# Performance work log

Measured on AMD Instinct MI355X. Metric: run time of the kernel, lower is better.

The kernel has to match this reference:

```python
import jax, jax.numpy as jnp
import numpy as np

EMB = 300; TOWERS = 6; LAYERS = 4; EPS = 1e-5; F_OUT = EMB // TOWERS  # 50
N_NODES = 3000; N_EDGES = 9000; N_GRAPHS = 64
NODE_VOCAB = 16; EDGE_VOCAB = 4


def _bn(x, g, b, m, v):
    # eval-mode BatchNorm1d with running stats
    return (x - m) * jax.lax.rsqrt(v + EPS) * g + b


def _forward(node_emb, edge_emb, W_edge, b_edge, W_pre, b_pre, W_post, b_post,
             W_lin, b_lin, bn_gamma, bn_beta, bn_mean, bn_var,
             head_w0, head_b0, gn0_gamma, gn0_beta, gn0_mean, gn0_var,
             head_w1, head_b1, gn1_gamma, gn1_beta, gn1_mean, gn1_var,
             head_w2, head_b2, x, edge_index, edge_attr, batch, num_graphs):
    N = x.shape[0]
    src, dst = edge_index[0], edge_index[1]
    h = node_emb[x]            # [N, D] node encoder (categorical embedding)
    e = edge_emb[edge_attr]    # [E, D] edge encoder
    cnt = jax.ops.segment_sum(jnp.ones(src.shape, h.dtype), dst, num_segments=N)
    deg = jnp.maximum(cnt, 1.0)
    log_deg = jnp.log(deg + 1.0)
    avg_log = jnp.mean(jnp.log(cnt + 1.0))  # PNA avg_deg['log'] of degree histogram
    amp = (log_deg / avg_log)[:, None, None]
    att = (avg_log / log_deg)[:, None, None]
    has_nb = (cnt > 0)[:, None, None]
    degc = deg[:, None, None]

    h_list = [h]
    for l in range(LAYERS):
        eproj = e @ W_edge[l] + b_edge[l]                        # [E, D]
        hcat = jnp.concatenate([h[dst], h[src], eproj], -1)      # [E, 3D] = [x_i, x_j, e]
        m = jnp.einsum('ef,tfd->etd', hcat, W_pre[l]) + b_pre[l]  # [E, T, D] per-tower pre-MLP
        s = jax.ops.segment_sum(m, dst, num_segments=N)
        mean = s / degc
        mn = jnp.where(has_nb, jax.ops.segment_min(m, dst, num_segments=N), 0.0)
        mx = jnp.where(has_nb, jax.ops.segment_max(m, dst, num_segments=N), 0.0)
        var = jax.ops.segment_sum(m * m, dst, num_segments=N) / degc - mean * mean
        std = jnp.sqrt(jax.nn.relu(var) + EPS)
        agg = jnp.concatenate([mean, mn, mx, std], -1)           # [N, T, 4D]
        agg = jnp.concatenate([agg, agg * amp, agg * att], -1)   # [N, T, 12D] scalers
        x_rep = jnp.broadcast_to(h[:, None, :], (N, TOWERS, EMB))
        post_in = jnp.concatenate([x_rep, agg], -1)              # [N, T, 13D]
        out = jnp.einsum('ntf,tfo->nto', post_in, W_post[l]) + b_post[l]  # [N, T, F_OUT]
        out = out.reshape(N, EMB) @ W_lin[l] + b_lin[l]
        out = _bn(out, bn_gamma[l], bn_beta[l], bn_mean[l], bn_var[l])
        if l < LAYERS - 1:
            out = jax.nn.relu(out)  # dropout is identity in eval mode
        h_list.append(out)
        h = out
    # JK='sum' exactly as in the original forward: sums h_list[0..num_layer-1]
    node_rep = h_list[0]
    for l in range(1, LAYERS):
        node_rep = node_rep + h_list[l]
    g = jax.ops.segment_sum(node_rep, batch, num_segments=num_graphs)  # global_add_pool
    g = jax.nn.relu(_bn(g @ head_w0 + head_b0, gn0_gamma, gn0_beta, gn0_mean, gn0_var))
    g = jax.nn.relu(_bn(g @ head_w1 + head_b1, gn1_gamma, gn1_beta, gn1_mean, gn1_var))
    return g @ head_w2 + head_b2


def setup_inputs() -> dict:
    key = jax.random.key(0)
    ks = jax.random.split(key, 16)
    D, T, L = EMB, TOWERS, LAYERS
    def rn(k, shape, s=0.05):
        return jax.random.normal(k, shape, dtype=jnp.float32) * s
    return {
        'x': jax.random.randint(ks[0], (N_NODES,), 0, NODE_VOCAB, dtype=jnp.int32),
        'edge_index': jax.random.randint(ks[1], (2, N_EDGES), 0, N_NODES, dtype=jnp.int32),
        'edge_attr': jax.random.randint(ks[2], (N_EDGES,), 0, EDGE_VOCAB, dtype=jnp.int32),
        'batch': jnp.sort(jax.random.randint(ks[3], (N_NODES,), 0, N_GRAPHS, dtype=jnp.int32)),
        'num_graphs': N_GRAPHS,
        'node_emb': rn(ks[4], (NODE_VOCAB, D), 1.0),
        'edge_emb': rn(ks[5], (EDGE_VOCAB, D), 1.0),
        'W_edge': rn(ks[6], (L, D, D)), 'b_edge': jnp.zeros((L, D), jnp.float32),
        'W_pre': rn(ks[7], (L, T, 3 * D, D)), 'b_pre': jnp.zeros((L, T, D), jnp.float32),
        'W_post': rn(ks[8], (L, T, 13 * D, F_OUT)), 'b_post': jnp.zeros((L, T, F_OUT), jnp.float32),
        'W_lin': rn(ks[9], (L, D, D)), 'b_lin': jnp.zeros((L, D), jnp.float32),
        'bn_gamma': jnp.ones((L, D), jnp.float32), 'bn_beta': jnp.zeros((L, D), jnp.float32),
        'bn_mean': jnp.zeros((L, D), jnp.float32), 'bn_var': jnp.ones((L, D), jnp.float32),
        'head_w0': rn(ks[10], (D, 2 * D)), 'head_b0': jnp.zeros((2 * D,), jnp.float32),
        'gn0_gamma': jnp.ones((2 * D,), jnp.float32), 'gn0_beta': jnp.zeros((2 * D,), jnp.float32),
        'gn0_mean': jnp.zeros((2 * D,), jnp.float32), 'gn0_var': jnp.ones((2 * D,), jnp.float32),
        'head_w1': rn(ks[11], (2 * D, D)), 'head_b1': jnp.zeros((D,), jnp.float32),
        'gn1_gamma': jnp.ones((D,), jnp.float32), 'gn1_beta': jnp.zeros((D,), jnp.float32),
        'gn1_mean': jnp.zeros((D,), jnp.float32), 'gn1_var': jnp.ones((D,), jnp.float32),
        'head_w2': rn(ks[12], (D, 1)), 'head_b2': jnp.zeros((1,), jnp.float32),
    }


def reference(x, edge_index, edge_attr, batch, num_graphs,
              node_emb, edge_emb, W_edge, b_edge, W_pre, b_pre, W_post, b_post,
              W_lin, b_lin, bn_gamma, bn_beta, bn_mean, bn_var,
              head_w0, head_b0, gn0_gamma, gn0_beta, gn0_mean, gn0_var,
              head_w1, head_b1, gn1_gamma, gn1_beta, gn1_mean, gn1_var,
              head_w2, head_b2):
    return _forward(node_emb, edge_emb, W_edge, b_edge, W_pre, b_pre, W_post, b_post,
                    W_lin, b_lin, bn_gamma, bn_beta, bn_mean, bn_var,
                    head_w0, head_b0, gn0_gamma, gn0_beta, gn0_mean, gn0_var,
                    head_w1, head_b1, gn1_gamma, gn1_beta, gn1_mean, gn1_var,
                    head_w2, head_b2, x, edge_index, edge_attr, batch, num_graphs)
```

## Files before the change

### kernel.cpp

```cpp
#include <hip/hip_runtime.h>
#include <math.h>

#define NN 3000
#define NE 9000
#define NG 64
#define D 300
#define NT 6
#define FO 50
#define EPSV 1e-5f
#define NB1 3900

__global__ void k_hist(const int* __restrict__ dst, int* __restrict__ cnt) {
    int e = blockIdx.x * blockDim.x + threadIdx.x;
    if (e < NE) atomicAdd(&cnt[dst[e]], 1);
}

__global__ __launch_bounds__(1024) void k_scan(
    const int* __restrict__ cnt, int* __restrict__ row_ptr, int* __restrict__ tmp_ptr,
    float* __restrict__ degf, float* __restrict__ ampv, float* __restrict__ attv) {
    __shared__ int s_part[1024];
    __shared__ float s_log[1024];
    int tid = threadIdx.x;
    int base = tid * 3;
    int c0 = 0, c1 = 0, c2 = 0; float lg = 0.f;
    if (base + 0 < NN) { c0 = cnt[base + 0]; lg += logf((float)c0 + 1.f); }
    if (base + 1 < NN) { c1 = cnt[base + 1]; lg += logf((float)c1 + 1.f); }
    if (base + 2 < NN) { c2 = cnt[base + 2]; lg += logf((float)c2 + 1.f); }
    s_part[tid] = c0 + c1 + c2;
    s_log[tid] = lg;
    __syncthreads();
    for (int off = 1; off < 1024; off <<= 1) {
        int v = (tid >= off) ? s_part[tid - off] : 0;
        __syncthreads();
        s_part[tid] += v;
        __syncthreads();
    }
    for (int off = 512; off > 0; off >>= 1) {
        if (tid < off) s_log[tid] += s_log[tid + off];
        __syncthreads();
    }
    float avg = s_log[0] / (float)NN;
    int run = (tid > 0) ? s_part[tid - 1] : 0;
    int cs[3] = {c0, c1, c2};
    for (int i = 0; i < 3; i++) {
        int n = base + i;
        if (n < NN) {
            row_ptr[n] = run; tmp_ptr[n] = run;
            int cc = cs[i];
            float dd = (float)(cc > 0 ? cc : 1);
            degf[n] = dd;
            float ld = logf(dd + 1.f);
            ampv[n] = ld / avg;
            attv[n] = avg / ld;
            run += cc;
        }
    }
    if (tid == 1023) row_ptr[NN] = s_part[1023];
}

__global__ void k_fill(const int* __restrict__ src, const int* __restrict__ dst,
                       const int* __restrict__ attr, int* __restrict__ tmp_ptr,
                       int2* __restrict__ edge_dat) {
    int e = blockIdx.x * blockDim.x + threadIdx.x;
    if (e < NE) {
        int d = dst[e];
        int p = atomicAdd(&tmp_ptr[d], 1);
        edge_dat[p] = make_int2(src[e], attr[e]);
    }
}

__global__ void k_embed(const int* __restrict__ x, const float* __restrict__ node_emb,
                        float* __restrict__ h, float* __restrict__ rep) {
    int i = blockIdx.x * blockDim.x + threadIdx.x;
    if (i < NN * D) {
        int n = i / D, d = i - n * D;
        float v = node_emb[x[n] * D + d];
        h[i] = v; rep[i] = v;
    }
}

__global__ void k_pack1(const float* __restrict__ W_pre, const float* __restrict__ W_post,
                        int l, float* __restrict__ Bp) {
    int idx = blockIdx.x * blockDim.x + threadIdx.x;
    if (idx >= 300 * NB1) return;
    int f = idx / NB1, j = idx - f * NB1;
    float v;
    if (j < 3600) {
        int s = j / 1800, r = j - s * 1800;
        int t = r / 300, d = r - t * 300;
        v = W_pre[(((size_t)(l * NT + t) * 900) + s * 300 + f) * 300 + d];
    } else {
        int jj = j - 3600;
        int t = jj / FO, o = jj - t * FO;
        v = W_post[((size_t)(l * NT + t) * 3900 + f) * FO + o];
    }
    Bp[idx] = v;
}

__global__ void k_packpost(const float* __restrict__ W_post, int l, float* __restrict__ Bp) {
    int idx = blockIdx.x * blockDim.x + threadIdx.x;
    if (idx >= NT * 1200 * 160) return;
    int t = idx / 192000, r = idx - t * 192000;
    int f = r / 160, c = r - f * 160;
    float v = 0.f;
    if (c < 150) {
        int k = c / FO, o = c - k * FO;
        v = W_post[((size_t)(l * NT + t) * 3900 + 300 + k * 1200 + f) * FO + o];
    }
    Bp[idx] = v;
}

__global__ void k_ep4(const float* __restrict__ edge_emb, const float* __restrict__ W_edge,
                      const float* __restrict__ b_edge, int l, float* __restrict__ ep4) {
    int idx = blockIdx.x * blockDim.x + threadIdx.x;
    if (idx >= 4 * 300) return;
    int a = idx / 300, f = idx - a * 300;
    float s = b_edge[l * 300 + f];
    for (int k = 0; k < 300; k++)
        s = fmaf(edge_emb[a * 300 + k], W_edge[((size_t)l * 300 + k) * 300 + f], s);
    ep4[idx] = s;
}

__global__ void k_ep_proj(const float* __restrict__ ep4, const float* __restrict__ W_pre,
                          const float* __restrict__ b_pre, int l, float* __restrict__ Ep) {
    int idx = blockIdx.x * blockDim.x + threadIdx.x;
    if (idx >= 4 * 1800) return;
    int a = idx / 1800, c = idx - a * 1800;
    int t = c / 300, d = c - t * 300;
    float s = b_pre[(l * NT + t) * 300 + d];
    for (int f = 0; f < 300; f++)
        s = fmaf(ep4[a * 300 + f], W_pre[(((size_t)(l * NT + t) * 900) + 600 + f) * 300 + d], s);
    Ep[idx] = s;
}

__global__ void k_pack_lin(const float* __restrict__ W_lin, const float* __restrict__ b_lin,
                           const float* __restrict__ gam, const float* __restrict__ bet,
                           const float* __restrict__ mu, const float* __restrict__ var,
                           int l, float* __restrict__ Wf, float* __restrict__ bf) {
    int idx = blockIdx.x * blockDim.x + threadIdx.x;
    if (idx >= 300 * 300) return;
    int f = idx / 300, j = idx - f * 300;
    float s = gam[l * 300 + j] * rsqrtf(var[l * 300 + j] + EPSV);
    Wf[idx] = W_lin[((size_t)l * 300 + f) * 300 + j] * s;
    if (f == 0) bf[j] = (b_lin[l * 300 + j] - mu[l * 300 + j]) * s + bet[l * 300 + j];
}

template <int EPI>
__global__ __launch_bounds__(256) void k_gemm(
    const float* __restrict__ A, int lda,
    const float* __restrict__ B, int ldb,
    float* __restrict__ C, int ldc,
    int M, int N, int K,
    const float* __restrict__ bias, float* __restrict__ rep,
    const float* __restrict__ gam, const float* __restrict__ bet,
    const float* __restrict__ mu, const float* __restrict__ var) {
    constexpr int BM = 64, BN = 64, BK = 16, LAS = BM + 4;
    __shared__ float As[BK * LAS];
    __shared__ float Bs[BK * BN];
    int tid = threadIdx.x;
    int tx = tid & 15, ty = tid >> 4;
    int bm = blockIdx.y * BM, bn = blockIdx.x * BN;
    int arow = tid >> 2;
    int akq = (tid & 3) * 4;
    int bj = tid & 63, bk0 = tid >> 6;
    float acc[4][4] = {};
    for (int k0 = 0; k0 < K; k0 += BK) {
        {
            float4 av = make_float4(0.f, 0.f, 0.f, 0.f);
            int grow = bm + arow;
            if (grow < M) {
                int gk = k0 + akq;
                if (gk + 3 < K) {
                    av = *(const float4*)&A[(size_t)grow * lda + gk];
                } else {
                    float t0 = (gk + 0 < K) ? A[(size_t)grow * lda + gk + 0] : 0.f;
                    float t1 = (gk + 1 < K) ? A[(size_t)grow * lda + gk + 1] : 0.f;
                    float t2 = (gk + 2 < K) ? A[(size_t)grow * lda + gk + 2] : 0.f;
                    float t3 = (gk + 3 < K) ? A[(size_t)grow * lda + gk + 3] : 0.f;
                    av = make_float4(t0, t1, t2, t3);
                }
            }
            As[(akq + 0) * LAS + arow] = av.x;
            As[(akq + 1) * LAS + arow] = av.y;
            As[(akq + 2) * LAS + arow] = av.z;
            As[(akq + 3) * LAS + arow] = av.w;
        }
        #pragma unroll
        for (int it = 0; it < 4; ++it) {
            int k = bk0 + it * 4;
            int gk = k0 + k, gj = bn + bj;
            float v = 0.f;
            if (gk < K && gj < N) v = B[(size_t)gk * ldb + gj];
            Bs[k * BN + bj] = v;
        }
        __syncthreads();
        #pragma unroll
        for (int kk = 0; kk < BK; ++kk) {
            float4 a = *(const float4*)&As[kk * LAS + ty * 4];
            float4 b = *(const float4*)&Bs[kk * BN + tx * 4];
            float ar[4] = {a.x, a.y, a.z, a.w};
            float br[4] = {b.x, b.y, b.z, b.w};
            #pragma unroll
            for (int i = 0; i < 4; i++)
                #pragma unroll
                for (int j = 0; j < 4; j++)
                    acc[i][j] = fmaf(ar[i], br[j], acc[i][j]);
        }
        __syncthreads();
    }
    #pragma unroll
    for (int i = 0; i < 4; i++) {
        int r = bm + ty * 4 + i;
        if (r >= M) continue;
        #pragma unroll
        for (int j = 0; j < 4; j++) {
            int c = bn + tx * 4 + j;
            if (c >= N) continue;
            float v = acc[i][j];
            if (EPI == 1) {
                v += bias[c];
                v = fmaxf(v, 0.f);
                C[(size_t)r * ldc + c] = v;
                rep[(size_t)r * ldc + c] += v;
            } else if (EPI == 2) {
                v += bias[c];
                v = (v - mu[c]) * rsqrtf(var[c] + EPSV) * gam[c] + bet[c];
                v = fmaxf(v, 0.f);
                C[(size_t)r * ldc + c] = v;
            } else {
                C[(size_t)r * ldc + c] = v;
            }
        }
    }
}

__global__ __launch_bounds__(256) void k_gemm1(const float* __restrict__ A,
                                               const float* __restrict__ B,
                                               float* __restrict__ C) {
    constexpr int BM = 128, BN = 128, BK = 16, LAS = BM + 4;
    constexpr int M = 3000, N = NB1, K = 300;
    __shared__ float As[BK * LAS];
    __shared__ float Bs[BK * BN];
    int tid = threadIdx.x;
    int tx = tid & 15, ty = tid >> 4;
    int bm = blockIdx.y * BM, bn = blockIdx.x * BN;
    float acc[8][8] = {};
    for (int k0 = 0; k0 < K; k0 += BK) {
        #pragma unroll
        for (int it = 0; it < 2; ++it) {
            int i = tid + it * 256;
            int row = i >> 2, kq = (i & 3) * 4;
            int grow = bm + row, gk = k0 + kq;
            float4 av = make_float4(0.f, 0.f, 0.f, 0.f);
            if (grow < M && gk < K) av = *(const float4*)&A[(size_t)grow * 300 + gk];
            As[(kq + 0) * LAS + row] = av.x;
            As[(kq + 1) * LAS + row] = av.y;
            As[(kq + 2) * LAS + row] = av.z;
            As[(kq + 3) * LAS + row] = av.w;
        }
        #pragma unroll
        for (int it = 0; it < 2; ++it) {
            int i = tid + it * 256;
            int k = i >> 5, c = (i & 31) * 4;
            int gk = k0 + k, gj = bn + c;
            float4 bv = make_float4(0.f, 0.f, 0.f, 0.f);
            if (gk < K && gj < N) bv = *(const float4*)&B[(size_t)gk * N + gj];
            *(float4*)&Bs[k * BN + c] = bv;
        }
        __syncthreads();
        #pragma unroll
        for (int kk = 0; kk < BK; ++kk) {
            float a[8], b[8];
            *(float4*)&a[0] = *(const float4*)&As[kk * LAS + ty * 8];
            *(float4*)&a[4] = *(const float4*)&As[kk * LAS + ty * 8 + 4];
            *(float4*)&b[0] = *(const float4*)&Bs[kk * BN + tx * 8];
            *(float4*)&b[4] = *(const float4*)&Bs[kk * BN + tx * 8 + 4];
            #pragma unroll
            for (int i = 0; i < 8; i++)
                #pragma unroll
                for (int j = 0; j < 8; j++)
                    acc[i][j] = fmaf(a[i], b[j], acc[i][j]);
        }
        __syncthreads();
    }
    int r0 = bm + ty * 8, c0 = bn + tx * 8;
    #pragma unroll
    for (int i = 0; i < 8; i++) {
        int r = r0 + i;
        if (r >= M) break;
        if (c0 + 8 <= N) {
            float4 v0 = make_float4(acc[i][0], acc[i][1], acc[i][2], acc[i][3]);
            float4 v1 = make_float4(acc[i][4], acc[i][5], acc[i][6], acc[i][7]);
            *(float4*)&C[(size_t)r * N + c0] = v0;
            *(float4*)&C[(size_t)r * N + c0 + 4] = v1;
        } else {
            #pragma unroll
            for (int j = 0; j < 8; j++)
                if (c0 + j < N) C[(size_t)r * N + c0 + j] = acc[i][j];
        }
    }
}

__global__ __launch_bounds__(256) void k_gemmp(const float* __restrict__ agg,
                                               const float* __restrict__ Bp,
                                               float* __restrict__ P) {
    constexpr int BM = 64, BN = 160, BK = 16, LAS = BM + 4, KC = 400;
    __shared__ float As[BK * LAS];
    __shared__ float Bs[BK * BN];
    int z = blockIdx.z;
    int t = z % 6, kc = z / 6;
    const float* A = agg + t * 1200 + kc * KC;
    const float* B = Bp + t * 192000 + kc * KC * 160;
    float* C = P + (size_t)z * 480000;
    int tid = threadIdx.x;
    int tx = tid & 15, ty = tid >> 4;
    int bm = blockIdx.y * BM;
    float acc[4][10] = {};
    for (int k0 = 0; k0 < KC; k0 += BK) {
        {
            int row = tid >> 2, kq = (tid & 3) * 4;
            int grow = bm + row;
            float4 av = make_float4(0.f, 0.f, 0.f, 0.f);
            if (grow < 3000) av = *(const float4*)&A[(size_t)grow * 7200 + k0 + kq];
            As[(kq + 0) * LAS + row] = av.x;
            As[(kq + 1) * LAS + row] = av.y;
            As[(kq + 2) * LAS + row] = av.z;
            As[(kq + 3) * LAS + row] = av.w;
        }
        #pragma unroll
        for (int it = 0; it < 3; ++it) {
            int i = tid + it * 256;
            if (i < 640) {
                int k = i / 40, c = (i - k * 40) * 4;
                *(float4*)&Bs[k * BN + c] = *(const float4*)&B[(size_t)(k0 + k) * 160 + c];
            }
        }
        __syncthreads();
        #pragma unroll
        for (int kk = 0; kk < BK; ++kk) {
            float a[4], b[10];
            *(float4*)&a[0] = *(const float4*)&As[kk * LAS + ty * 4];
            #pragma unroll
            for (int j = 0; j < 10; j++) b[j] = Bs[kk * BN + tx * 10 + j];
            #pragma unroll
            for (int i = 0; i < 4; i++)
                #pragma unroll
                for (int j = 0; j < 10; j++)
                    acc[i][j] = fmaf(a[i], b[j], acc[i][j]);
        }
        __syncthreads();
    }
    int r0 = bm + ty * 4, c0 = tx * 10;
    #pragma unroll
    for (int i = 0; i < 4; i++) {
        int r = r0 + i;
        if (r >= 3000) break;
        #pragma unroll
        for (int j = 0; j < 10; j++)
            C[(size_t)r * 160 + c0 + j] = acc[i][j];
    }
}

__global__ __launch_bounds__(256) void k_agg(
    const float* __restrict__ HH, const float* __restrict__ Ep,
    const int* __restrict__ row_ptr, const int2* __restrict__ edge_dat,
    const float* __restrict__ degf, const int* __restrict__ xv, int use_vocab,
    float* __restrict__ agg) {
    int n = blockIdx.x;
    int e0 = row_ptr[n], e1 = row_ptr[n + 1];
    int cnt = e1 - e0;
    float cntf = (float)cnt;
    float deg = degf[n];
    float inv_deg = 1.f / deg;
    int nrow = use_vocab ? xv[n] : n;
    const float* hdrow = HH + (size_t)nrow * NB1;
    for (int c4 = threadIdx.x; c4 < 450; c4 += 256) {
        int c = c4 * 4;
        float sx = 0.f, sy = 0.f, sz = 0.f, sw = 0.f;
        float qx = 0.f, qy = 0.f, qz = 0.f, qw = 0.f;
        float mnx = INFINITY, mny = INFINITY, mnz = INFINITY, mnw = INFINITY;
        float mxx = -INFINITY, mxy = -INFINITY, mxz = -INFINITY, mxw = -INFINITY;
        for (int e = e0; e < e1; ++e) {
            int2 sa = edge_dat[e];
            int srow = use_vocab ? xv[sa.x] : sa.x;
            float4 hv = *(const float4*)&HH[(size_t)srow * NB1 + 1800 + c];
            float4 ev = *(const float4*)&Ep[(size_t)sa.y * 1800 + c];
            float vx = hv.x + ev.x, vy = hv.y + ev.y, vz = hv.z + ev.z, vw = hv.w + ev.w;
            sx += vx; sy += vy; sz += vz; sw += vw;
            qx = fmaf(vx, vx, qx); qy = fmaf(vy, vy, qy);
            qz = fmaf(vz, vz, qz); qw = fmaf(vw, vw, qw);
            mnx = fminf(mnx, vx); mny = fminf(mny, vy);
            mnz = fminf(mnz, vz); mnw = fminf(mnw, vw);
            mxx = fmaxf(mxx, vx); mxy = fmaxf(mxy, vy);
            mxz = fmaxf(mxz, vz); mxw = fmaxf(mxw, vw);
        }
        float4 hd = *(const float4*)&hdrow[c];
        float4 mean, mnv, mxv, stdv;
        {
            mean.x = (cntf * hd.x + sx) * inv_deg;
            mean.y = (cntf * hd.y + sy) * inv_deg;
            mean.z = (cntf * hd.z + sz) * inv_deg;
            mean.w = (cntf * hd.w + sw) * inv_deg;
            if (cnt > 0) {
                mnv.x = hd.x + mnx; mnv.y = hd.y + mny; mnv.z = hd.z + mnz; mnv.w = hd.w + mnw;
                mxv.x = hd.x + mxx; mxv.y = hd.y + mxy; mxv.z = hd.z + mxz; mxv.w = hd.w + mxw;
            } else {
                mnv = make_float4(0.f, 0.f, 0.f, 0.f);
                mxv = make_float4(0.f, 0.f, 0.f, 0.f);
            }
            float vrx = (cntf * hd.x * hd.x + 2.f * hd.x * sx + qx) * inv_deg - mean.x * mean.x;
            float vry = (cntf * hd.y * hd.y + 2.f * hd.y * sy + qy) * inv_deg - mean.y * mean.y;
            float vrz = (cntf * hd.z * hd.z + 2.f * hd.z * sz + qz) * inv_deg - mean.z * mean.z;
            float vrw = (cntf * hd.w * hd.w + 2.f * hd.w * sw + qw) * inv_deg - mean.w * mean.w;
            stdv.x = sqrtf(fmaxf(vrx, 0.f) + EPSV);
            stdv.y = sqrtf(fmaxf(vry, 0.f) + EPSV);
            stdv.z = sqrtf(fmaxf(vrz, 0.f) + EPSV);
            stdv.w = sqrtf(fmaxf(vrw, 0.f) + EPSV);
        }
        int t = c / 300, d = c - t * 300;
        float* arow = agg + (size_t)n * 7200 + (size_t)t * 1200 + d;
        *(float4*)&arow[0]   = mean;
        *(float4*)&arow[300] = mnv;
        *(float4*)&arow[600] = mxv;
        *(float4*)&arow[900] = stdv;
    }
}

__global__ void k_combine(const float* __restrict__ HH, const float* __restrict__ P,
                          const float* __restrict__ ampv, const float* __restrict__ attv,
                          const float* __restrict__ b_post_l, const int* __restrict__ xv,
                          int use_vocab, float* __restrict__ out_pre) {
    int i = blockIdx.x * blockDim.x + threadIdx.x;
    if (i >= NN * D) return;
    int n = i / D, j = i - n * D;
    int t = j / FO, o = j - t * FO;
    int nrow = use_vocab ? xv[n] : n;
    float p1 = 0.f, p2 = 0.f, p3 = 0.f;
    #pragma unroll
    for (int kc = 0; kc < 3; kc++) {
        const float* Pr = P + ((size_t)(kc * 6 + t) * 3000 + n) * 160;
        p1 += Pr[o];
        p2 += Pr[50 + o];
        p3 += Pr[100 + o];
    }
    float v = HH[(size_t)nrow * NB1 + 3600 + j] + p1 + ampv[n] * p2 + attv[n] * p3
              + b_post_l[t * FO + o];
    out_pre[i] = v;
}

__global__ __launch_bounds__(256) void k_pool(const float* __restrict__ rep,
                                              const int* __restrict__ batch,
                                              float* __restrict__ g) {
    __shared__ int s_lo, s_hi;
    int b = blockIdx.x;
    if (threadIdx.x == 0) {
        int lo = 0, hi = NN;
        while (lo < hi) { int m = (lo + hi) >> 1; if (batch[m] < b) lo = m + 1; else hi = m; }
        s_lo = lo;
        int lo2 = lo, hi2 = NN;
        while (lo2 < hi2) { int m = (lo2 + hi2) >> 1; if (batch[m] < b + 1) lo2 = m + 1; else hi2 = m; }
        s_hi = lo2;
    }
    __syncthreads();
    int lo = s_lo, hi = s_hi;
    for (int j = threadIdx.x; j < D; j += blockDim.x) {
        float s = 0.f;
        for (int n = lo; n < hi; ++n) s += rep[(size_t)n * D + j];
        g[b * D + j] = s;
    }
}

__global__ void k_head2(const float* __restrict__ g2, const float* __restrict__ w2,
                        const float* __restrict__ b2, float* __restrict__ out) {
    int b = blockIdx.x;
    int tid = threadIdx.x;
    float s = 0.f;
    for (int k = tid; k < 300; k += 64) s += g2[b * 300 + k] * w2[k];
    for (int off = 32; off; off >>= 1) s += __shfl_down(s, off, 64);
    if (tid == 0) out[b] = s + b2[0];
}

extern "C" void kernel_launch(void* const* d_in, const int* in_sizes, int n_in,
                              void* d_out, int out_size, void* d_ws, size_t ws_size,
                              hipStream_t stream) {
    const int* x      = (const int*)d_in[0];
    const int* ei     = (const int*)d_in[1];
    const int* src    = ei;
    const int* dst    = ei + NE;
    const int* eattr  = (const int*)d_in[2];
    const int* batch  = (const int*)d_in[3];
    const float* node_emb = (const float*)d_in[5];
    const float* edge_emb = (const float*)d_in[6];
    const float* W_edge   = (const float*)d_in[7];
    const float* b_edge   = (const float*)d_in[8];
    const float* W_pre    = (const float*)d_in[9];
    const float* b_pre    = (const float*)d_in[10];
    const float* W_post   = (const float*)d_in[11];
    const float* b_post   = (const float*)d_in[12];
    const float* W_lin    = (const float*)d_in[13];
    const float* b_lin    = (const float*)d_in[14];
    const float* bn_gamma = (const float*)d_in[15];
    const float* bn_beta  = (const float*)d_in[16];
    const float* bn_mean  = (const float*)d_in[17];
    const float* bn_var   = (const float*)d_in[18];
    const float* head_w0  = (const float*)d_in[19];
    const float* head_b0  = (const float*)d_in[20];
    const float* gn0_g    = (const float*)d_in[21];
    const float* gn0_b    = (const float*)d_in[22];
    const float* gn0_m    = (const float*)d_in[23];
    const float* gn0_v    = (const float*)d_in[24];
    const float* head_w1  = (const float*)d_in[25];
    const float* head_b1  = (const float*)d_in[26];
    const float* gn1_g    = (const float*)d_in[27];
    const float* gn1_b    = (const float*)d_in[28];
    const float* gn1_m    = (const float*)d_in[29];
    const float* gn1_v    = (const float*)d_in[30];
    const float* head_w2  = (const float*)d_in[31];
    const float* head_b2  = (const float*)d_in[32];
    float* out = (float*)d_out;

    unsigned char* base = (unsigned char*)d_ws;
    size_t off = 0;
    auto alloc = [&](size_t bytes) -> void* {
        void* p = base + off;
        off += (bytes + 255) & ~(size_t)255;
        return p;
    };
    int*   cnt      = (int*)alloc(NN * 4);
    int*   row_ptr  = (int*)alloc((NN + 1) * 4);
    int*   tmp_ptr  = (int*)alloc(NN * 4);
    int2*  edge_dat = (int2*)alloc(NE * 8);
    float* degf     = (float*)alloc(NN * 4);
    float* ampv     = (float*)alloc(NN * 4);
    float* attv     = (float*)alloc(NN * 4);
    float* h        = (float*)alloc((size_t)NN * D * 4);
    float* rep      = (float*)alloc((size_t)NN * D * 4);
    float* HsHd     = (float*)alloc((size_t)NN * NB1 * 4);
    float* Bpack1   = (float*)alloc((size_t)300 * NB1 * 4);
    float* ep4      = (float*)alloc(4 * 300 * 4);
    float* Ep       = (float*)alloc(4 * 1800 * 4);
    float* agg      = (float*)alloc((size_t)NN * 7200 * 4);
    float* Bpost    = (float*)alloc((size_t)NT * 1200 * 160 * 4);
    float* P        = (float*)alloc((size_t)18 * 3000 * 160 * 4);
    float* out_pre  = (float*)alloc((size_t)NN * D * 4);
    float* Wlin_f   = (float*)alloc((size_t)300 * 300 * 4);
    float* b_f      = (float*)alloc(300 * 4);
    float* gsum     = (float*)alloc(NG * D * 4);
    float* gbuf0    = (float*)alloc(NG * 600 * 4);
    float* gbuf1    = (float*)alloc(NG * 300 * 4);
    (void)ws_size; (void)n_in; (void)in_sizes; (void)out_size;

    hipMemsetAsync(cnt, 0, NN * 4, stream);
    k_hist<<<(NE + 255) / 256, 256, 0, stream>>>(dst, cnt);
    k_scan<<<1, 1024, 0, stream>>>(cnt, row_ptr, tmp_ptr, degf, ampv, attv);
    k_fill<<<(NE + 255) / 256, 256, 0, stream>>>(src, dst, eattr, tmp_ptr, edge_dat);
    k_embed<<<(NN * D + 255) / 256, 256, 0, stream>>>(x, node_emb, h, rep);

    for (int l = 0; l < 3; ++l) {
        const float* Ain = (l == 0) ? node_emb : h;
        int M = (l == 0) ? 16 : NN;
        int uv = (l == 0) ? 1 : 0;

        k_pack1<<<(300 * NB1 + 255) / 256, 256, 0, stream>>>(W_pre, W_post, l, Bpack1);
        if (l == 0) {
            k_gemm<0><<<dim3((NB1 + 63) / 64, 1, 1), 256, 0, stream>>>(
                Ain, 300, Bpack1, NB1, HsHd, NB1, M, NB1, 300,
                nullptr, nullptr, nullptr, nullptr, nullptr, nullptr);
        } else {
            k_gemm1<<<dim3((NB1 + 127) / 128, 24, 1), 256, 0, stream>>>(Ain, Bpack1, HsHd);
        }

        k_ep4<<<(1200 + 255) / 256, 256, 0, stream>>>(edge_emb, W_edge, b_edge, l, ep4);
        k_ep_proj<<<(7200 + 255) / 256, 256, 0, stream>>>(ep4, W_pre, b_pre, l, Ep);

        k_agg<<<NN, 256, 0, stream>>>(HsHd, Ep, row_ptr, edge_dat, degf, x, uv, agg);

        k_packpost<<<(NT * 1200 * 160 + 255) / 256, 256, 0, stream>>>(W_post, l, Bpost);
        k_gemmp<<<dim3(1, 47, 18), 256, 0, stream>>>(agg, Bpost, P);

        k_combine<<<(NN * D + 255) / 256, 256, 0, stream>>>(
            HsHd, P, ampv, attv, b_post + l * NT * FO, x, uv, out_pre);

        k_pack_lin<<<(300 * 300 + 255) / 256, 256, 0, stream>>>(
            W_lin, b_lin, bn_gamma, bn_beta, bn_mean, bn_var, l, Wlin_f, b_f);
        k_gemm<1><<<dim3(5, 47, 1), 256, 0, stream>>>(
            out_pre, 300, Wlin_f, 300, h, 300, NN, 300, 300,
            b_f, rep, nullptr, nullptr, nullptr, nullptr);
    }

    k_pool<<<NG, 256, 0, stream>>>(rep, batch, gsum);
    k_gemm<2><<<dim3(10, 1, 1), 256, 0, stream>>>(
        gsum, 300, head_w0, 600, gbuf0, 600, NG, 600, 300,
        head_b0, nullptr, gn0_g, gn0_b, gn0_m, gn0_v);
    k_gemm<2><<<dim3(5, 1, 1), 256, 0, stream>>>(
        gbuf0, 600, head_w1, 300, gbuf1, 300, NG, 300, 600,
        head_b1, nullptr, gn1_g, gn1_b, gn1_m, gn1_v);
    k_head2<<<NG, 64, 0, stream>>>(gbuf1, head_w2, head_b2, out);
}
```

Measured before the change: 1.317 ms.

## Double-buffer shared memory in GEMMs, shrink gemm1 tile, split post GEMM K finer

```diff
diff --git a/kernel.cpp b/kernel.cpp
--- a/kernel.cpp
+++ b/kernel.cpp
@@ -237,55 +237,71 @@
 __global__ __launch_bounds__(256) void k_gemm1(const float* __restrict__ A,
                                                const float* __restrict__ B,
                                                float* __restrict__ C) {
-    constexpr int BM = 128, BN = 128, BK = 16, LAS = BM + 4;
+    constexpr int BM = 64, BN = 128, BK = 16, LAS = BM + 4;
     constexpr int M = 3000, N = NB1, K = 300;
-    __shared__ float As[BK * LAS];
-    __shared__ float Bs[BK * BN];
+    constexpr int NSTEP = (K + BK - 1) / BK;
+    __shared__ float As[2][BK * LAS];
+    __shared__ float Bs[2][BK * BN];
     int tid = threadIdx.x;
     int tx = tid & 15, ty = tid >> 4;
     int bm = blockIdx.y * BM, bn = blockIdx.x * BN;
-    float acc[8][8] = {};
-    for (int k0 = 0; k0 < K; k0 += BK) {
-        #pragma unroll
-        for (int it = 0; it < 2; ++it) {
-            int i = tid + it * 256;
-            int row = i >> 2, kq = (i & 3) * 4;
-            int grow = bm + row, gk = k0 + kq;
-            float4 av = make_float4(0.f, 0.f, 0.f, 0.f);
-            if (grow < M && gk < K) av = *(const float4*)&A[(size_t)grow * 300 + gk];
-            As[(kq + 0) * LAS + row] = av.x;
-            As[(kq + 1) * LAS + row] = av.y;
-            As[(kq + 2) * LAS + row] = av.z;
-            As[(kq + 3) * LAS + row] = av.w;
-        }
-        #pragma unroll
-        for (int it = 0; it < 2; ++it) {
-            int i = tid + it * 256;
-            int k = i >> 5, c = (i & 31) * 4;
-            int gk = k0 + k, gj = bn + c;
-            float4 bv = make_float4(0.f, 0.f, 0.f, 0.f);
-            if (gk < K && gj < N) bv = *(const float4*)&B[(size_t)gk * N + gj];
-            *(float4*)&Bs[k * BN + c] = bv;
-        }
-        __syncthreads();
+    int arow = tid >> 2, akq = (tid & 3) * 4;
+    int grow = bm + arow;
+    bool am = grow < M;
+    int kB = tid >> 5, cB = (tid & 31) * 4;
+    int gj = bn + cB;
+    bool bj = gj < N;
+    float4 rA, rB0, rB1;
+    float acc[4][8] = {};
+
+    auto ldA = [&](int k0) {
+        int gk = k0 + akq;
+        rA = (am && gk < K) ? *(const float4*)&A[(size_t)grow * 300 + gk]
+                            : make_float4(0.f, 0.f, 0.f, 0.f);
+    };
+    auto ldB = [&](int k0) {
+        int g0 = k0 + kB, g1 = k0 + kB + 8;
+        rB0 = (g0 < K && bj) ? *(const float4*)&B[(size_t)g0 * N + gj]
+                             : make_float4(0.f, 0.f, 0.f, 0.f);
+        rB1 = (g1 < K && bj) ? *(const float4*)&B[(size_t)g1 * N + gj]
+                             : make_float4(0.f, 0.f, 0.f, 0.f);
+    };
+    auto stW = [&](int b) {
+        As[b][(akq + 0) * LAS + arow] = rA.x;
+        As[b][(akq + 1) * LAS + arow] = rA.y;
+        As[b][(akq + 2) * LAS + arow] = rA.z;
+        As[b][(akq + 3) * LAS + arow] = rA.w;
+        *(float4*)&Bs[b][kB * BN + cB] = rB0;
+        *(float4*)&Bs[b][(kB + 8) * BN + cB] = rB1;
+    };
+
+    ldA(0); ldB(0); stW(0);
+    __syncthreads();
+    int buf = 0;
+    for (int step = 0; step < NSTEP; ++step) {
+        if (step + 1 < NSTEP) { ldA((step + 1) * BK); ldB((step + 1) * BK); }
         #pragma unroll
         for (int kk = 0; kk < BK; ++kk) {
-            float a[8], b[8];
-            *(float4*)&a[0] = *(const float4*)&As[kk * LAS + ty * 8];
-            *(float4*)&a[4] = *(const float4*)&As[kk * LAS + ty * 8 + 4];
-            *(float4*)&b[0] = *(const float4*)&Bs[kk * BN + tx * 8];
-            *(float4*)&b[4] = *(const float4*)&Bs[kk * BN + tx * 8 + 4];
+            float a[4], b[8];
+            *(float4*)&a[0] = *(const float4*)&As[buf][kk * LAS + ty * 4];
+            *(float4*)&b[0] = *(const float4*)&Bs[buf][kk * BN + tx * 8];
+            *(float4*)&b[4] = *(const float4*)&Bs[buf][kk * BN + tx * 8 + 4];
             #pragma unroll
-            for (int i = 0; i < 8; i++)
+            for (int i = 0; i < 4; i++)
                 #pragma unroll
                 for (int j = 0; j < 8; j++)
                     acc[i][j] = fmaf(a[i], b[j], acc[i][j]);
         }
-        __syncthreads();
-    }
-    int r0 = bm + ty * 8, c0 = bn + tx * 8;
+        if (step + 1 < NSTEP) {
+            int nbuf = buf ^ 1;
+            stW(nbuf);
+            __syncthreads();
+            buf = nbuf;
+        }
+    }
+    int r0 = bm + ty * 4, c0 = bn + tx * 8;
     #pragma unroll
-    for (int i = 0; i < 8; i++) {
+    for (int i = 0; i < 4; i++) {
         int r = r0 + i;
         if (r >= M) break;
         if (c0 + 8 <= N) {
@@ -304,9 +320,10 @@
 __global__ __launch_bounds__(256) void k_gemmp(const float* __restrict__ agg,
                                                const float* __restrict__ Bp,
                                                float* __restrict__ P) {
-    constexpr int BM = 64, BN = 160, BK = 16, LAS = BM + 4, KC = 400;
-    __shared__ float As[BK * LAS];
-    __shared__ float Bs[BK * BN];
+    constexpr int BM = 64, BN = 160, BK = 16, LAS = BM + 4, KC = 240;
+    constexpr int NSTEP = KC / BK;
+    __shared__ float As[2][BK * LAS];
+    __shared__ float Bs[2][BK * BN];
     int z = blockIdx.z;
     int t = z % 6, kc = z / 6;
     const float* A = agg + t * 1200 + kc * KC;
@@ -315,40 +332,59 @@
     int tid = threadIdx.x;
     int tx = tid & 15, ty = tid >> 4;
     int bm = blockIdx.y * BM;
+    int arow = tid >> 2, akq = (tid & 3) * 4;
+    int grow = bm + arow;
+    bool am = grow < 3000;
+    const float* Arow = A + (size_t)grow * 7200 + akq;
+    int kB0 = tid / 40;        int cB0 = (tid - kB0 * 40) * 4;
+    int i1 = tid + 256; int kB1 = i1 / 40; int cB1 = (i1 - kB1 * 40) * 4;
+    int i2 = tid + 512; int kB2 = i2 / 40; int cB2 = (i2 - kB2 * 40) * 4;
+    bool b2 = i2 < 640;
+    float4 rA, rB0, rB1, rB2;
     float acc[4][10] = {};
-    for (int k0 = 0; k0 < KC; k0 += BK) {
-        {
-            int row = tid >> 2, kq = (tid & 3) * 4;
-            int grow = bm + row;
-            float4 av = make_float4(0.f, 0.f, 0.f, 0.f);
-            if (grow < 3000) av = *(const float4*)&A[(size_t)grow * 7200 + k0 + kq];
-            As[(kq + 0) * LAS + row] = av.x;
-            As[(kq + 1) * LAS + row] = av.y;
-            As[(kq + 2) * LAS + row] = av.z;
-            As[(kq + 3) * LAS + row] = av.w;
-        }
-        #pragma unroll
-        for (int it = 0; it < 3; ++it) {
-            int i = tid + it * 256;
-            if (i < 640) {
-                int k = i / 40, c = (i - k * 40) * 4;
-                *(float4*)&Bs[k * BN + c] = *(const float4*)&B[(size_t)(k0 + k) * 160 + c];
-            }
-        }
-        __syncthreads();
+
+    auto ld = [&](int k0) {
+        rA = am ? *(const float4*)&Arow[k0] : make_float4(0.f, 0.f, 0.f, 0.f);
+        rB0 = *(const float4*)&B[(size_t)(k0 + kB0) * 160 + cB0];
+        rB1 = *(const float4*)&B[(size_t)(k0 + kB1) * 160 + cB1];
+        if (b2) rB2 = *(const float4*)&B[(size_t)(k0 + kB2) * 160 + cB2];
+    };
+    auto stW = [&](int b) {
+        As[b][(akq + 0) * LAS + arow] = rA.x;
+        As[b][(akq + 1) * LAS + arow] = rA.y;
+        As[b][(akq + 2) * LAS + arow] = rA.z;
+        As[b][(akq + 3) * LAS + arow] = rA.w;
+        *(float4*)&Bs[b][kB0 * BN + cB0] = rB0;
+        *(float4*)&Bs[b][kB1 * BN + cB1] = rB1;
+        if (b2) *(float4*)&Bs[b][kB2 * BN + cB2] = rB2;
+    };
+
+    ld(0); stW(0);
+    __syncthreads();
+    int buf = 0;
+    for (int step = 0; step < NSTEP; ++step) {
+        if (step + 1 < NSTEP) ld((step + 1) * BK);
         #pragma unroll
         for (int kk = 0; kk < BK; ++kk) {
             float a[4], b[10];
-            *(float4*)&a[0] = *(const float4*)&As[kk * LAS + ty * 4];
-            #pragma unroll
-            for (int j = 0; j < 10; j++) b[j] = Bs[kk * BN + tx * 10 + j];
+            *(float4*)&a[0] = *(const float4*)&As[buf][kk * LAS + ty * 4];
+            *(float2*)&b[0] = *(const float2*)&Bs[buf][kk * BN + tx * 10 + 0];
+            *(float2*)&b[2] = *(const float2*)&Bs[buf][kk * BN + tx * 10 + 2];
+            *(float2*)&b[4] = *(const float2*)&Bs[buf][kk * BN + tx * 10 + 4];
+            *(float2*)&b[6] = *(const float2*)&Bs[buf][kk * BN + tx * 10 + 6];
+            *(float2*)&b[8] = *(const float2*)&Bs[buf][kk * BN + tx * 10 + 8];
             #pragma unroll
             for (int i = 0; i < 4; i++)
                 #pragma unroll
                 for (int j = 0; j < 10; j++)
                     acc[i][j] = fmaf(a[i], b[j], acc[i][j]);
         }
-        __syncthreads();
+        if (step + 1 < NSTEP) {
+            int nbuf = buf ^ 1;
+            stW(nbuf);
+            __syncthreads();
+            buf = nbuf;
+        }
     }
     int r0 = bm + ty * 4, c0 = tx * 10;
     #pragma unroll
@@ -437,7 +473,7 @@
     int nrow = use_vocab ? xv[n] : n;
     float p1 = 0.f, p2 = 0.f, p3 = 0.f;
     #pragma unroll
-    for (int kc = 0; kc < 3; kc++) {
+    for (int kc = 0; kc < 5; kc++) {
         const float* Pr = P + ((size_t)(kc * 6 + t) * 3000 + n) * 160;
         p1 += Pr[o];
         p2 += Pr[50 + o];
@@ -541,7 +577,7 @@
     float* Ep       = (float*)alloc(4 * 1800 * 4);
     float* agg      = (float*)alloc((size_t)NN * 7200 * 4);
     float* Bpost    = (float*)alloc((size_t)NT * 1200 * 160 * 4);
-    float* P        = (float*)alloc((size_t)18 * 3000 * 160 * 4);
+    float* P        = (float*)alloc((size_t)30 * 3000 * 160 * 4);
     float* out_pre  = (float*)alloc((size_t)NN * D * 4);
     float* Wlin_f   = (float*)alloc((size_t)300 * 300 * 4);
     float* b_f      = (float*)alloc(300 * 4);
@@ -567,7 +603,7 @@
                 Ain, 300, Bpack1, NB1, HsHd, NB1, M, NB1, 300,
                 nullptr, nullptr, nullptr, nullptr, nullptr, nullptr);
         } else {
-            k_gemm1<<<dim3((NB1 + 127) / 128, 24, 1), 256, 0, stream>>>(Ain, Bpack1, HsHd);
+            k_gemm1<<<dim3((NB1 + 127) / 128, 47, 1), 256, 0, stream>>>(Ain, Bpack1, HsHd);
         }
 
         k_ep4<<<(1200 + 255) / 256, 256, 0, stream>>>(edge_emb, W_edge, b_edge, l, ep4);
@@ -576,7 +612,7 @@
         k_agg<<<NN, 256, 0, stream>>>(HsHd, Ep, row_ptr, edge_dat, degf, x, uv, agg);
 
         k_packpost<<<(NT * 1200 * 160 + 255) / 256, 256, 0, stream>>>(W_post, l, Bpost);
-        k_gemmp<<<dim3(1, 47, 18), 256, 0, stream>>>(agg, Bpost, P);
+        k_gemmp<<<dim3(1, 47, 30), 256, 0, stream>>>(agg, Bpost, P);
 
         k_combine<<<(NN * D + 255) / 256, 256, 0, stream>>>(
             HsHd, P, ampv, attv, b_post + l * NT * FO, x, uv, out_pre);
```

New measurement: 1.516 ms. +15.1%, slower.
